# Optimization experiments

Measured on AMD Instinct MI355X. Metric: run time of the kernel, lower is better.

The kernel has to match this reference:

```python
import jax, jax.numpy as jnp
import numpy as np

B, S, HID = 2, 2048, 4096
NUM_HEADS, NUM_KV_HEADS, HEAD_DIM = 32, 8, 128
KV_SIZE = HID * NUM_KV_HEADS // NUM_HEADS  # 1024


def setup_inputs() -> dict:
    key = jax.random.key(0)
    ks = jax.random.split(key, 5)
    x = jax.random.normal(ks[0], (B, S, HID), dtype=jnp.float32)
    wq = jax.random.normal(ks[1], (HID, HID), dtype=jnp.float32) * 0.02
    wk = jax.random.normal(ks[2], (HID, KV_SIZE), dtype=jnp.float32) * 0.02
    wv = jax.random.normal(ks[3], (HID, KV_SIZE), dtype=jnp.float32) * 0.02
    wo = jax.random.normal(ks[4], (KV_SIZE, HID), dtype=jnp.float32) * 0.02
    return {"x": x, "wq": wq, "wk": wk, "wv": wv, "wo": wo}


def reference(x, wq, wk, wv, wo):
    b, s, _ = x.shape
    g = NUM_HEADS // NUM_KV_HEADS  # num_head_groups
    q = x @ wq  # [b, s, hid]
    k = x @ wk  # [b, s, kv_size]
    v = x @ wv  # [b, s, kv_size]
    # 'b s (h d) -> b h s d' with h = num_heads
    q = q.reshape(b, s, NUM_HEADS, HEAD_DIM).transpose(0, 2, 1, 3)
    # 'b s (h d) -> b h d s' with h = num_kv_heads
    k = k.reshape(b, s, NUM_KV_HEADS, HEAD_DIM).transpose(0, 2, 3, 1)
    # 'b s (h d) -> b h s d'
    v = v.reshape(b, s, NUM_KV_HEADS, HEAD_DIM).transpose(0, 2, 1, 3)
    # 'b (h g) s d -> b g h s d' with g = num_head_groups, h = num_kv_heads
    q = q.reshape(b, NUM_KV_HEADS, g, s, HEAD_DIM).transpose(0, 2, 1, 3, 4)
    # NOTE: faithful to source - g is contracted (summed) here, it does not
    # appear in the output subscripts.
    scores = jnp.einsum('bghqd,bhdk->bhqk', q, k) / jnp.sqrt(
        jnp.asarray(HEAD_DIM, dtype=x.dtype))
    scores = jax.nn.softmax(scores, axis=-1)
    values = jnp.einsum('bhqk,bhkd->bhqd', scores, v)  # [b, h_kv, s, d]
    values = values.transpose(0, 2, 1, 3).reshape(b, s, KV_SIZE)
    return values @ wo  # [b, s, hid]
```

## Files before the change

kernel.cpp:

```cpp
#include <hip/hip_runtime.h>
#include <stdint.h>

#define S 2048
#define HID 4096
#define NKV 8
#define HD 128
#define KV 1024
#define BATCH 2
#define NQKV 3072
#define MROWS 4096

typedef __attribute__((ext_vector_type(4))) float f32x4;
typedef __attribute__((ext_vector_type(8))) __bf16 bf16x8;
typedef __attribute__((ext_vector_type(8))) unsigned short ushort8;
typedef __attribute__((ext_vector_type(4))) unsigned short ushort4_t;
typedef __attribute__((ext_vector_type(4))) float float4_t;

__device__ __forceinline__ unsigned short f2bf(float f) {
    unsigned int u = __builtin_bit_cast(unsigned int, f);
    u += 0x7fffu + ((u >> 16) & 1u);
    return (unsigned short)(u >> 16);
}
__device__ __forceinline__ float bf2f(unsigned short s) {
    unsigned int u = ((unsigned int)s) << 16;
    return __builtin_bit_cast(float, u);
}

__device__ __forceinline__ void gl2lds16(const void* g, void* l) {
    __builtin_amdgcn_global_load_lds(
        (const __attribute__((address_space(1))) void*)(uintptr_t)(g),
        (__attribute__((address_space(3))) void*)(uintptr_t)(l),
        16, 0, 0);
}

__global__ __launch_bounds__(256) void castx_kernel(const float* __restrict__ x,
                                                    unsigned short* __restrict__ xb) {
    int i = (blockIdx.x * 256 + threadIdx.x) * 4;
    float4_t v = *(const float4_t*)&x[i];
    ushort4_t o;
    o.x = f2bf(v.x); o.y = f2bf(v.y); o.z = f2bf(v.z); o.w = f2bf(v.w);
    *(ushort4_t*)&xb[i] = o;
}

__global__ __launch_bounds__(256) void wcat_kernel(const float* __restrict__ wq,
                                                   const float* __restrict__ wk,
                                                   const float* __restrict__ wv,
                                                   unsigned short* __restrict__ WcatT) {
    __shared__ float T[64 * 65];
    const int tid = threadIdx.x;
    const int k0 = blockIdx.x * 64;
    const int n0 = blockIdx.y * 64;
    const float scale = 0.088388347648318447f;
#pragma unroll
    for (int i = 0; i < 16; i++) {
        int kl = (tid >> 6) + i * 4;
        int nl = tid & 63;
        int k = k0 + kl, n = n0 + nl;
        float v;
        if (n < KV) {
            int kvh = n >> 7, d = n & 127;
            const float* p = wq + (size_t)k * HID + kvh * 512 + d;
            v = (p[0] + p[128] + p[256] + p[384]) * scale;
        } else if (n < 2048) {
            v = wk[(size_t)k * KV + (n - KV)];
        } else {
            v = wv[(size_t)k * KV + (n - 2048)];
        }
        T[kl * 65 + nl] = v;
    }
    __syncthreads();
#pragma unroll
    for (int i = 0; i < 16; i++) {
        int nl = (tid >> 6) + i * 4;
        int kl = tid & 63;
        WcatT[(size_t)(n0 + nl) * HID + k0 + kl] = f2bf(T[kl * 65 + nl]);
    }
}

__global__ __launch_bounds__(256) void wot_kernel(const float* __restrict__ wo,
                                                  unsigned short* __restrict__ woT) {
    __shared__ float T[64 * 65];
    const int tid = threadIdx.x;
    const int k0 = blockIdx.x * 64;
    const int n0 = blockIdx.y * 64;
#pragma unroll
    for (int i = 0; i < 16; i++) {
        int kl = (tid >> 6) + i * 4, nl = tid & 63;
        T[kl * 65 + nl] = wo[(size_t)(k0 + kl) * HID + n0 + nl];
    }
    __syncthreads();
#pragma unroll
    for (int i = 0; i < 16; i++) {
        int nl = (tid >> 6) + i * 4, kl = tid & 63;
        woT[(size_t)(n0 + nl) * KV + k0 + kl] = f2bf(T[kl * 65 + nl]);
    }
}

template <int OUT_BF16>
__global__ __launch_bounds__(256) void gemm_bt(const unsigned short* __restrict__ A,
                                               const unsigned short* __restrict__ Bt,
                                               void* __restrict__ Cv,
                                               int M, int N, int K) {
    __shared__ unsigned short Asl[128 * 32];
    __shared__ unsigned short Bsl[128 * 32];
    const int tid = threadIdx.x;
    const int lane = tid & 63;
    const int wave = tid >> 6;
    const int lm = lane & 15;
    const int quad = lane >> 4;
    const int wm = (wave >> 1) << 6;
    const int wn = (wave & 1) << 6;
    const int m0 = blockIdx.y * 128;
    const int n0 = blockIdx.x * 128;

    f32x4 acc[4][4] = {};

    const int r0 = tid >> 2;
    const int kc = tid & 3;
    const int gsw = kc ^ ((r0 >> 1) & 3);
    const int rsw = (lm >> 1) & 3;
    const size_t Abase = (size_t)(m0 + r0) * K + gsw * 8;
    const size_t Bbase = (size_t)(n0 + r0) * K + gsw * 8;
    unsigned short* As0 = &Asl[tid * 8];
    unsigned short* As1 = &Asl[(tid + 256) * 8];
    unsigned short* Bs0 = &Bsl[tid * 8];
    unsigned short* Bs1 = &Bsl[(tid + 256) * 8];

    for (int k0 = 0; k0 < K; k0 += 32) {
        gl2lds16(A + Abase + k0, As0);
        gl2lds16(A + Abase + (size_t)64 * K + k0, As1);
        gl2lds16(Bt + Bbase + k0, Bs0);
        gl2lds16(Bt + Bbase + (size_t)64 * K + k0, Bs1);
        __syncthreads();
        bf16x8 af[4], bfr[4];
#pragma unroll
        for (int i = 0; i < 4; i++)
            af[i] = *(const bf16x8*)&Asl[(wm + i * 16 + lm) * 32 + (quad ^ rsw) * 8];
#pragma unroll
        for (int j = 0; j < 4; j++)
            bfr[j] = *(const bf16x8*)&Bsl[(wn + j * 16 + lm) * 32 + (quad ^ rsw) * 8];
#pragma unroll
        for (int i = 0; i < 4; i++)
#pragma unroll
            for (int j = 0; j < 4; j++)
                acc[i][j] = __builtin_amdgcn_mfma_f32_16x16x32_bf16(af[i], bfr[j], acc[i][j], 0, 0, 0);
        __syncthreads();
    }
#pragma unroll
    for (int i = 0; i < 4; i++) {
        const int row = m0 + wm + i * 16 + quad * 4;
#pragma unroll
        for (int j = 0; j < 4; j++) {
            const int col = n0 + wn + j * 16 + lm;
#pragma unroll
            for (int r = 0; r < 4; r++) {
                if (OUT_BF16)
                    ((unsigned short*)Cv)[(size_t)(row + r) * N + col] = f2bf(acc[i][j][r]);
                else
                    ((float*)Cv)[(size_t)(row + r) * N + col] = acc[i][j][r];
            }
        }
    }
}

__global__ __launch_bounds__(256) void vt_kernel(const unsigned short* __restrict__ QKV,
                                                 unsigned short* __restrict__ Vt) {
    __shared__ unsigned short T[128 * 136];
    const int tid = threadIdx.x;
    const int st = blockIdx.x;
    const int bh = blockIdx.y;
    const int b = bh >> 3, h = bh & 7;
#pragma unroll
    for (int it = 0; it < 8; it++) {
        int chunk = tid + it * 256;
        int s = chunk >> 4, cc = chunk & 15;
        ushort8 v = *(const ushort8*)&QKV[(size_t)(b * S + st * 128 + s) * NQKV + 2048 + h * HD + cc * 8];
        *(ushort8*)&T[s * 136 + cc * 8] = v;
    }
    __syncthreads();
#pragma unroll
    for (int it = 0; it < 8; it++) {
        int chunk = tid + it * 256;
        int d = chunk >> 4, scc = chunk & 15;
        ushort8 o;
#pragma unroll
        for (int j = 0; j < 8; j++) o[j] = T[(scc * 8 + j) * 136 + d];
        *(ushort8*)&Vt[(size_t)((b * NKV + h) * HD + d) * S + st * 128 + scc * 8] = o;
    }
}

__global__ __launch_bounds__(256, 1) void attn_kernel(const unsigned short* __restrict__ QKV,
                                                      const unsigned short* __restrict__ Vt,
                                                      unsigned short* __restrict__ Oout) {
    __shared__ unsigned short Ks[64 * 128];
    __shared__ unsigned short Vs[128 * 64];
    __shared__ unsigned short Ps[128 * 64];
    const int tid = threadIdx.x;
    const int lane = tid & 63, wave = tid >> 6;
    const int lm = lane & 15, quad = lane >> 4;
    const int sw = lm & 7;
    const int qt = blockIdx.x;
    const int h = blockIdx.y;
    const int b = blockIdx.z;
    const int qrow0 = qt * 128 + wave * 32;

    bf16x8 qf[2][4];
#pragma unroll
    for (int rt = 0; rt < 2; rt++)
#pragma unroll
        for (int ks = 0; ks < 4; ks++) {
            size_t off = (size_t)(b * S + qrow0 + rt * 16 + lm) * NQKV + h * HD + ks * 32 + quad * 8;
            qf[rt][ks] = *(const bf16x8*)&QKV[off];
        }

    float lsum[2][4] = {};
    f32x4 oacc[2][8] = {};

    const int krow = tid >> 2, kc4 = tid & 3;
    const int vrow = tid >> 1, vc2 = tid & 1;
    const unsigned short* Kg0 = QKV + (size_t)(b * S) * NQKV + KV + h * HD + kc4 * 32;
    const unsigned short* Vg0 = Vt + (size_t)((b * NKV + h) * HD + vrow) * S + vc2 * 32;

    ushort8 kreg[4], vreg[4];
    {
        const unsigned short* kg = Kg0 + (size_t)krow * NQKV;
        const unsigned short* vg = Vg0;
#pragma unroll
        for (int j = 0; j < 4; j++) kreg[j] = *(const ushort8*)(kg + j * 8);
#pragma unroll
        for (int j = 0; j < 4; j++) vreg[j] = *(const ushort8*)(vg + j * 8);
    }

    for (int kt = 0; kt < 32; kt++) {
        __syncthreads();
#pragma unroll
        for (int j = 0; j < 4; j++)
            *(ushort8*)&Ks[krow * 128 + ((kc4 * 4 + j) ^ (krow & 7)) * 8] = kreg[j];
#pragma unroll
        for (int j = 0; j < 4; j++)
            *(ushort8*)&Vs[vrow * 64 + ((vc2 * 4 + j) ^ (vrow & 7)) * 8] = vreg[j];
        __syncthreads();
        if (kt < 31) {
            const unsigned short* kg = Kg0 + (size_t)((kt + 1) * 64 + krow) * NQKV;
            const unsigned short* vg = Vg0 + (kt + 1) * 64;
#pragma unroll
            for (int j = 0; j < 4; j++) kreg[j] = *(const ushort8*)(kg + j * 8);
#pragma unroll
            for (int j = 0; j < 4; j++) vreg[j] = *(const ushort8*)(vg + j * 8);
        }

        f32x4 sc[2][4] = {};
#pragma unroll
        for (int ks = 0; ks < 4; ks++)
#pragma unroll
            for (int ct = 0; ct < 4; ct++) {
                bf16x8 kf = *(const bf16x8*)&Ks[(ct * 16 + lm) * 128 + ((ks * 4 + quad) ^ sw) * 8];
                sc[0][ct] = __builtin_amdgcn_mfma_f32_16x16x32_bf16(qf[0][ks], kf, sc[0][ct], 0, 0, 0);
                sc[1][ct] = __builtin_amdgcn_mfma_f32_16x16x32_bf16(qf[1][ks], kf, sc[1][ct], 0, 0, 0);
            }

#pragma unroll
        for (int rt = 0; rt < 2; rt++)
#pragma unroll
            for (int ct = 0; ct < 4; ct++)
#pragma unroll
                for (int r = 0; r < 4; r++) {
                    float p = __expf(fminf(sc[rt][ct][r], 60.f));
                    unsigned short pb = f2bf(p);
                    lsum[rt][r] += bf2f(pb);
                    int prow = wave * 32 + rt * 16 + quad * 4 + r;
                    int pcol = ct * 16 + lm;
                    Ps[prow * 64 + (((pcol >> 3) ^ (prow & 7)) * 8) + (pcol & 7)] = pb;
                }

#pragma unroll
        for (int ks = 0; ks < 2; ks++) {
            bf16x8 af0 = *(const bf16x8*)&Ps[(wave * 32 + lm) * 64 + ((ks * 4 + quad) ^ sw) * 8];
            bf16x8 af1 = *(const bf16x8*)&Ps[(wave * 32 + 16 + lm) * 64 + ((ks * 4 + quad) ^ sw) * 8];
#pragma unroll
            for (int dt = 0; dt < 8; dt++) {
                bf16x8 vf = *(const bf16x8*)&Vs[(dt * 16 + lm) * 64 + ((ks * 4 + quad) ^ sw) * 8];
                oacc[0][dt] = __builtin_amdgcn_mfma_f32_16x16x32_bf16(af0, vf, oacc[0][dt], 0, 0, 0);
                oacc[1][dt] = __builtin_amdgcn_mfma_f32_16x16x32_bf16(af1, vf, oacc[1][dt], 0, 0, 0);
            }
        }
    }

#pragma unroll
    for (int rt = 0; rt < 2; rt++)
#pragma unroll
        for (int r = 0; r < 4; r++) {
            float v = lsum[rt][r];
            v += __shfl_xor(v, 8);
            v += __shfl_xor(v, 4);
            v += __shfl_xor(v, 2);
            v += __shfl_xor(v, 1);
            lsum[rt][r] = v;
        }
#pragma unroll
    for (int rt = 0; rt < 2; rt++)
#pragma unroll
        for (int dt = 0; dt < 8; dt++)
#pragma unroll
            for (int r = 0; r < 4; r++) {
                int row = b * S + qt * 128 + wave * 32 + rt * 16 + quad * 4 + r;
                int col = h * HD + dt * 16 + lm;
                Oout[(size_t)row * KV + col] = f2bf(oacc[rt][dt][r] / lsum[rt][r]);
            }
}

extern "C" void kernel_launch(void* const* d_in, const int* in_sizes, int n_in,
                              void* d_out, int out_size, void* d_ws, size_t ws_size,
                              hipStream_t stream) {
    (void)in_sizes; (void)n_in; (void)out_size; (void)ws_size;
    const float* x  = (const float*)d_in[0];
    const float* wq = (const float*)d_in[1];
    const float* wk = (const float*)d_in[2];
    const float* wv = (const float*)d_in[3];
    const float* wo = (const float*)d_in[4];
    float* out = (float*)d_out;
    char* ws = (char*)d_ws;

    unsigned short* xb    = (unsigned short*)(ws);
    unsigned short* WcatT = (unsigned short*)(ws + 33554432);
    unsigned short* woT   = (unsigned short*)(ws + 33554432 + 25165824);
    unsigned short* QKV   = (unsigned short*)(ws + 67108864);
    unsigned short* Vt    = (unsigned short*)(ws);
    unsigned short* AttnO = (unsigned short*)(ws + 8388608);

    castx_kernel<<<16384, 256, 0, stream>>>(x, xb);
    wcat_kernel<<<dim3(64, 48), 256, 0, stream>>>(wq, wk, wv, WcatT);
    wot_kernel<<<dim3(16, 64), 256, 0, stream>>>(wo, woT);
    gemm_bt<1><<<dim3(NQKV / 128, MROWS / 128), 256, 0, stream>>>(xb, WcatT, QKV, MROWS, NQKV, HID);
    vt_kernel<<<dim3(16, 16), 256, 0, stream>>>(QKV, Vt);
    attn_kernel<<<dim3(16, NKV, BATCH), 256, 0, stream>>>(QKV, Vt, AttnO);
    gemm_bt<0><<<dim3(HID / 128, MROWS / 128), 256, 0, stream>>>(AttnO, woT, out, MROWS, HID, KV);
}
```

Before: 459.3 us.

## Halve attention query tile to 64 rows and double grid for occupancy

The attention kernel now processes 64 query rows per block (16 per wave) instead of 128, doubling the grid from 256 to 512 blocks and allowing two blocks per CU via launch bounds. The QK MFMA is transposed (K as A operand), so each lane holds scores for one query column and can write P to shared memory as 4-element vectors, with the row sum reduced across quads at the end. The intent is to fill more CUs with the small 256-block grid and cut register and LDS pressure. The cost is that each K/V tile is loaded twice as often per query row, raising global and LDS traffic.

```diff
diff --git a/kernel.cpp b/kernel.cpp
--- a/kernel.cpp
+++ b/kernel.cpp
@@ -189,12 +189,12 @@
     }
 }
 
-__global__ __launch_bounds__(256, 1) void attn_kernel(const unsigned short* __restrict__ QKV,
+__global__ __launch_bounds__(256, 2) void attn_kernel(const unsigned short* __restrict__ QKV,
                                                       const unsigned short* __restrict__ Vt,
                                                       unsigned short* __restrict__ Oout) {
     __shared__ unsigned short Ks[64 * 128];
     __shared__ unsigned short Vs[128 * 64];
-    __shared__ unsigned short Ps[128 * 64];
+    __shared__ unsigned short Ps[64 * 64];
     const int tid = threadIdx.x;
     const int lane = tid & 63, wave = tid >> 6;
     const int lm = lane & 15, quad = lane >> 4;
@@ -202,19 +202,17 @@
     const int qt = blockIdx.x;
     const int h = blockIdx.y;
     const int b = blockIdx.z;
-    const int qrow0 = qt * 128 + wave * 32;
-
-    bf16x8 qf[2][4];
-#pragma unroll
-    for (int rt = 0; rt < 2; rt++)
-#pragma unroll
-        for (int ks = 0; ks < 4; ks++) {
-            size_t off = (size_t)(b * S + qrow0 + rt * 16 + lm) * NQKV + h * HD + ks * 32 + quad * 8;
-            qf[rt][ks] = *(const bf16x8*)&QKV[off];
-        }
-
-    float lsum[2][4] = {};
-    f32x4 oacc[2][8] = {};
+    const int qrow0 = qt * 64 + wave * 16;
+
+    bf16x8 qf[4];
+#pragma unroll
+    for (int ks = 0; ks < 4; ks++) {
+        size_t off = (size_t)(b * S + qrow0 + lm) * NQKV + h * HD + ks * 32 + quad * 8;
+        qf[ks] = *(const bf16x8*)&QKV[off];
+    }
+
+    float lsum = 0.f;
+    f32x4 oacc[8] = {};
 
     const int krow = tid >> 2, kc4 = tid & 3;
     const int vrow = tid >> 1, vc2 = tid & 1;
@@ -224,11 +222,10 @@
     ushort8 kreg[4], vreg[4];
     {
         const unsigned short* kg = Kg0 + (size_t)krow * NQKV;
-        const unsigned short* vg = Vg0;
 #pragma unroll
         for (int j = 0; j < 4; j++) kreg[j] = *(const ushort8*)(kg + j * 8);
 #pragma unroll
-        for (int j = 0; j < 4; j++) vreg[j] = *(const ushort8*)(vg + j * 8);
+        for (int j = 0; j < 4; j++) vreg[j] = *(const ushort8*)(Vg0 + j * 8);
     }
 
     for (int kt = 0; kt < 32; kt++) {
@@ -249,64 +246,53 @@
             for (int j = 0; j < 4; j++) vreg[j] = *(const ushort8*)(vg + j * 8);
         }
 
-        f32x4 sc[2][4] = {};
+        f32x4 sc[4] = {};
 #pragma unroll
         for (int ks = 0; ks < 4; ks++)
 #pragma unroll
-            for (int ct = 0; ct < 4; ct++) {
-                bf16x8 kf = *(const bf16x8*)&Ks[(ct * 16 + lm) * 128 + ((ks * 4 + quad) ^ sw) * 8];
-                sc[0][ct] = __builtin_amdgcn_mfma_f32_16x16x32_bf16(qf[0][ks], kf, sc[0][ct], 0, 0, 0);
-                sc[1][ct] = __builtin_amdgcn_mfma_f32_16x16x32_bf16(qf[1][ks], kf, sc[1][ct], 0, 0, 0);
+            for (int t = 0; t < 4; t++) {
+                bf16x8 kf = *(const bf16x8*)&Ks[(t * 16 + lm) * 128 + ((ks * 4 + quad) ^ sw) * 8];
+                sc[t] = __builtin_amdgcn_mfma_f32_16x16x32_bf16(kf, qf[ks], sc[t], 0, 0, 0);
             }
 
 #pragma unroll
-        for (int rt = 0; rt < 2; rt++)
-#pragma unroll
-            for (int ct = 0; ct < 4; ct++)
-#pragma unroll
-                for (int r = 0; r < 4; r++) {
-                    float p = __expf(fminf(sc[rt][ct][r], 60.f));
-                    unsigned short pb = f2bf(p);
-                    lsum[rt][r] += bf2f(pb);
-                    int prow = wave * 32 + rt * 16 + quad * 4 + r;
-                    int pcol = ct * 16 + lm;
-                    Ps[prow * 64 + (((pcol >> 3) ^ (prow & 7)) * 8) + (pcol & 7)] = pb;
-                }
+        for (int t = 0; t < 4; t++) {
+            ushort4_t pb4;
+#pragma unroll
+            for (int r = 0; r < 4; r++) {
+                float p = __expf(fminf(sc[t][r], 60.f));
+                pb4[r] = f2bf(p);
+                lsum += bf2f(pb4[r]);
+            }
+            int c = t * 2 + (quad >> 1);
+            *(ushort4_t*)&Ps[(wave * 16 + lm) * 64 + ((c ^ sw) * 8) + (quad & 1) * 4] = pb4;
+        }
 
 #pragma unroll
         for (int ks = 0; ks < 2; ks++) {
-            bf16x8 af0 = *(const bf16x8*)&Ps[(wave * 32 + lm) * 64 + ((ks * 4 + quad) ^ sw) * 8];
-            bf16x8 af1 = *(const bf16x8*)&Ps[(wave * 32 + 16 + lm) * 64 + ((ks * 4 + quad) ^ sw) * 8];
+            bf16x8 af = *(const bf16x8*)&Ps[(wave * 16 + lm) * 64 + ((ks * 4 + quad) ^ sw) * 8];
 #pragma unroll
             for (int dt = 0; dt < 8; dt++) {
                 bf16x8 vf = *(const bf16x8*)&Vs[(dt * 16 + lm) * 64 + ((ks * 4 + quad) ^ sw) * 8];
-                oacc[0][dt] = __builtin_amdgcn_mfma_f32_16x16x32_bf16(af0, vf, oacc[0][dt], 0, 0, 0);
-                oacc[1][dt] = __builtin_amdgcn_mfma_f32_16x16x32_bf16(af1, vf, oacc[1][dt], 0, 0, 0);
+                oacc[dt] = __builtin_amdgcn_mfma_f32_16x16x32_bf16(af, vf, oacc[dt], 0, 0, 0);
             }
         }
     }
 
-#pragma unroll
-    for (int rt = 0; rt < 2; rt++)
+    lsum += __shfl_xor(lsum, 16);
+    lsum += __shfl_xor(lsum, 32);
+    float l4[4];
+#pragma unroll
+    for (int r = 0; r < 4; r++) l4[r] = __shfl(lsum, quad * 4 + r);
+
+#pragma unroll
+    for (int dt = 0; dt < 8; dt++)
 #pragma unroll
         for (int r = 0; r < 4; r++) {
-            float v = lsum[rt][r];
-            v += __shfl_xor(v, 8);
-            v += __shfl_xor(v, 4);
-            v += __shfl_xor(v, 2);
-            v += __shfl_xor(v, 1);
-            lsum[rt][r] = v;
-        }
-#pragma unroll
-    for (int rt = 0; rt < 2; rt++)
-#pragma unroll
-        for (int dt = 0; dt < 8; dt++)
-#pragma unroll
-            for (int r = 0; r < 4; r++) {
-                int row = b * S + qt * 128 + wave * 32 + rt * 16 + quad * 4 + r;
-                int col = h * HD + dt * 16 + lm;
-                Oout[(size_t)row * KV + col] = f2bf(oacc[rt][dt][r] / lsum[rt][r]);
-            }
+            int row = b * S + qt * 64 + wave * 16 + quad * 4 + r;
+            int col = h * HD + dt * 16 + lm;
+            Oout[(size_t)row * KV + col] = f2bf(oacc[dt][r] / l4[r]);
+        }
 }
 
 extern "C" void kernel_launch(void* const* d_in, const int* in_sizes, int n_in,
@@ -333,6 +319,6 @@
     wot_kernel<<<dim3(16, 64), 256, 0, stream>>>(wo, woT);
     gemm_bt<1><<<dim3(NQKV / 128, MROWS / 128), 256, 0, stream>>>(xb, WcatT, QKV, MROWS, NQKV, HID);
     vt_kernel<<<dim3(16, 16), 256, 0, stream>>>(QKV, Vt);
-    attn_kernel<<<dim3(16, NKV, BATCH), 256, 0, stream>>>(QKV, Vt, AttnO);
+    attn_kernel<<<dim3(32, NKV, BATCH), 256, 0, stream>>>(QKV, Vt, AttnO);
     gemm_bt<0><<<dim3(HID / 128, MROWS / 128), 256, 0, stream>>>(AttnO, woT, out, MROWS, HID, KV);
 }
```

Result: no change. 460.6 us (+0.3%).
